# Performance work log

Measured on AMD Instinct MI355X. Metric: run time of the kernel, lower is better.

## Reference

```python
import jax, jax.numpy as jnp
import numpy as np
from jax import lax

B, T, D = 2, 1024, 2048
HK, HV = 8, 16          # num key heads / num value heads
DK, DV = 128, 128       # head dims
KW = 4                  # conv kernel size
EPS = 1e-6
KEY_DIM = HK * DK
VALUE_DIM = HV * DV
CONV_DIM = 2 * KEY_DIM + VALUE_DIM


def setup_inputs() -> dict:
    key = jax.random.key(0)
    ks = jax.random.split(key, 9)
    w = lambda k, shape, s=0.02: jax.random.normal(k, shape, jnp.float32) * s
    return {
        'hidden_states': jax.random.normal(ks[0], (B, T, D), jnp.float32),
        'W_qkv': w(ks[1], (D, CONV_DIM)),
        'W_z': w(ks[2], (D, VALUE_DIM)),
        'W_b': w(ks[3], (D, HV)),
        'W_a': w(ks[4], (D, HV)),
        'conv_w': w(ks[5], (CONV_DIM, KW), 0.5),
        'dt_bias': jnp.ones((HV,), jnp.float32),
        'A_log': jnp.log(jax.random.uniform(ks[6], (HV,), jnp.float32, 1e-3, 16.0)),
        'norm_weight': jnp.ones((DV,), jnp.float32),
        'W_out': w(ks[7], (VALUE_DIM, D)),
    }


def _causal_conv_silu(x, w):
    # x: [B, C, T], w: [C, K] depthwise causal conv + SiLU (causal_conv1d_fn)
    k = w.shape[1]
    xp = jnp.pad(x, ((0, 0), (0, 0), (k - 1, 0)))
    y = sum(w[:, j][None, :, None] * xp[:, :, j:j + x.shape[2]] for j in range(k))
    return jax.nn.silu(y)


def _l2norm(x):
    return x * lax.rsqrt(jnp.sum(x * x, -1, keepdims=True) + 1e-6)


def reference(hidden_states, W_qkv, W_z, W_b, W_a, conv_w, dt_bias, A_log,
              norm_weight, W_out):
    Bb, Tt, _ = hidden_states.shape
    mixed = hidden_states @ W_qkv                       # [B,T,conv_dim]
    mixed = _causal_conv_silu(mixed.transpose(0, 2, 1), conv_w).transpose(0, 2, 1)
    q, k, v = jnp.split(mixed, [KEY_DIM, 2 * KEY_DIM], axis=-1)
    q = q.reshape(Bb, Tt, HK, DK)
    k = k.reshape(Bb, Tt, HK, DK)
    v = v.reshape(Bb, Tt, HV, DV)
    z = (hidden_states @ W_z).reshape(Bb, Tt, HV, DV)
    beta = jax.nn.sigmoid(hidden_states @ W_b)          # [B,T,HV]
    g = -jnp.exp(A_log) * jax.nn.softplus(hidden_states @ W_a + dt_bias)  # [B,T,HV]

    rep = HV // HK  # GQA: repeat_interleave q,k heads
    q = jnp.repeat(q, rep, axis=2)
    k = jnp.repeat(k, rep, axis=2)
    q = _l2norm(q) * (DK ** -0.5)                       # use_qk_l2norm + scale
    k = _l2norm(k)

    # gated delta-rule recurrence (fp32 state), scanned over time
    qs = q.transpose(1, 0, 2, 3)   # [T,B,HV,DK]
    ks = k.transpose(1, 0, 2, 3)
    vs = v.transpose(1, 0, 2, 3)   # [T,B,HV,DV]
    gs = g.transpose(1, 0, 2)      # [T,B,HV]
    bs = beta.transpose(1, 0, 2)

    def step(S, inp):
        qt, kt, vt, gt, bt = inp
        S = S * jnp.exp(gt)[..., None, None]                          # decay
        v_adj = (vt - jnp.einsum('bhk,bhkv->bhv', kt, S)) * bt[..., None]
        S = S + kt[..., None] * v_adj[..., None, :]                   # rank-1 delta update
        o = jnp.einsum('bhk,bhkv->bhv', qt, S)
        return S, o

    S0 = jnp.zeros((Bb, HV, DK, DV), jnp.float32)
    _, o = lax.scan(step, S0, (qs, ks, vs, gs, bs))
    o = o.transpose(1, 0, 2, 3)                         # [B,T,HV,DV]

    # gated RMSNorm over head_v_dim
    var = jnp.mean(o * o, -1, keepdims=True)
    o = o * lax.rsqrt(var + EPS) * norm_weight
    o = o * jax.nn.silu(z)

    return o.reshape(Bb, Tt, VALUE_DIM) @ W_out         # [B,T,D]
```

## Files before the change

kernel.cpp:

```cpp
#include <hip/hip_runtime.h>
#include <hip/hip_bf16.h>

#define B_ 2
#define T_ 1024
#define D_ 2048
#define HK_ 8
#define HV_ 16
#define DK_ 128
#define DV_ 128
#define KEY_DIM_ 1024
#define VALUE_DIM_ 2048
#define CONV_DIM_ 4096
#define BT_ 2048
#define NCH_ 16
#define CL_ 64

typedef __attribute__((ext_vector_type(8))) short short8;
typedef __attribute__((ext_vector_type(4))) float f32x4;

__device__ __forceinline__ short f2bf(float x) {
  __hip_bfloat16 h = __float2bfloat16(x);
  return *reinterpret_cast<short*>(&h);
}
__device__ __forceinline__ float bf2f(short u) {
  unsigned int x = ((unsigned int)(unsigned short)u) << 16;
  return __int_as_float(x);
}

#define GLOAD_LDS16(g, l)                                             \
  __builtin_amdgcn_global_load_lds(                                   \
      (const __attribute__((address_space(1))) void*)(g),             \
      (__attribute__((address_space(3))) void*)(l), 16, 0, 0)

__global__ void cast_plain(const float* __restrict__ in, short* __restrict__ out, int n4) {
  int i = blockIdx.x * blockDim.x + threadIdx.x;
  if (i < n4) {
    float4 v = ((const float4*)in)[i];
    short4 o;
    o.x = f2bf(v.x); o.y = f2bf(v.y); o.z = f2bf(v.z); o.w = f2bf(v.w);
    ((short4*)out)[i] = o;
  }
}

__global__ void transpose_cast(const float* __restrict__ W, short* __restrict__ WT, int R, int C) {
  __shared__ float tile[32][33];
  int tx = threadIdx.x, ty = threadIdx.y;
  int x = blockIdx.x * 32 + tx;
#pragma unroll
  for (int j = 0; j < 4; ++j) {
    int r = blockIdx.y * 32 + ty + j * 8;
    tile[ty + j * 8][tx] = W[(long)r * C + x];
  }
  __syncthreads();
  int ro = blockIdx.y * 32 + tx;
#pragma unroll
  for (int j = 0; j < 4; ++j) {
    int co = blockIdx.x * 32 + ty + j * 8;
    WT[(long)co * R + ro] = f2bf(tile[tx][ty + j * 8]);
  }
}

__global__ void interleave_ba(const float* __restrict__ Wb, const float* __restrict__ Wa,
                              float* __restrict__ Wba32) {
  int i = blockIdx.x * 256 + threadIdx.x;
  int c = i & 31, k = i >> 5;
  Wba32[i] = (c < 16) ? Wb[k * 16 + c] : Wa[k * 16 + (c - 16)];
}

__global__ __launch_bounds__(256) void gemm128_split(const short* __restrict__ A,
                                                     const short* __restrict__ Bt,
                                                     float* __restrict__ C0,
                                                     float* __restrict__ C1,
                                                     int N0, int N1, int K) {
  __shared__ short As[128 * 32];
  __shared__ short Bs[128 * 32];
  int m0 = blockIdx.y * 128, n0 = blockIdx.x * 128;
  int tid = threadIdx.x;
  int wave = tid >> 6, lane = tid & 63;
  int wm = (wave >> 1) * 64, wn = (wave & 1) * 64;
  int quad = lane >> 4, l16 = lane & 15;
  f32x4 acc[4][4] = {};

  int ar = tid >> 2;
  int ac = (tid & 3) * 8;
  const short* Ag0 = A + (long)(m0 + ar) * K + ac;
  const short* Ag1 = A + (long)(m0 + 64 + ar) * K + ac;
  const short* Bg0 = Bt + (long)(n0 + ar) * K + ac;
  const short* Bg1 = Bt + (long)(n0 + 64 + ar) * K + ac;
  short* lA0 = As + tid * 8;
  short* lA1 = As + 64 * 32 + tid * 8;
  short* lB0 = Bs + tid * 8;
  short* lB1 = Bs + 64 * 32 + tid * 8;

  for (int k0 = 0; k0 < K; k0 += 32) {
    GLOAD_LDS16(Ag0 + k0, lA0);
    GLOAD_LDS16(Ag1 + k0, lA1);
    GLOAD_LDS16(Bg0 + k0, lB0);
    GLOAD_LDS16(Bg1 + k0, lB1);
    __syncthreads();

    short8 af[4], bf_[4];
#pragma unroll
    for (int i = 0; i < 4; ++i) af[i] = *(const short8*)(As + (wm + i * 16 + l16) * 32 + quad * 8);
#pragma unroll
    for (int j = 0; j < 4; ++j) bf_[j] = *(const short8*)(Bs + (wn + j * 16 + l16) * 32 + quad * 8);
#pragma unroll
    for (int i = 0; i < 4; ++i)
#pragma unroll
      for (int j = 0; j < 4; ++j)
        acc[i][j] = __builtin_amdgcn_mfma_f32_16x16x32_bf16(af[i], bf_[j], acc[i][j], 0, 0, 0);
    __syncthreads();
  }

  float* Cw; int ldc, cb;
  if (n0 < N0) { Cw = C0; ldc = N0; cb = n0; }
  else         { Cw = C1; ldc = N1; cb = n0 - N0; }
#pragma unroll
  for (int i = 0; i < 4; ++i)
#pragma unroll
    for (int j = 0; j < 4; ++j)
#pragma unroll
      for (int r = 0; r < 4; ++r) {
        int row = m0 + wm + i * 16 + quad * 4 + r;
        int colx = cb + wn + j * 16 + l16;
        Cw[(long)row * ldc + colx] = acc[i][j][r];
      }
}

__global__ __launch_bounds__(256) void gemm128_ks(const short* __restrict__ A,
                                                  const short* __restrict__ Bt,
                                                  float* __restrict__ Cp,
                                                  int M, int N, int K) {
  __shared__ short As[128 * 32];
  __shared__ short Bs[128 * 32];
  int m0 = blockIdx.y * 128, n0 = blockIdx.x * 128;
  int kh = K >> 1;
  int kbeg = blockIdx.z * kh;
  int tid = threadIdx.x;
  int wave = tid >> 6, lane = tid & 63;
  int wm = (wave >> 1) * 64, wn = (wave & 1) * 64;
  int quad = lane >> 4, l16 = lane & 15;
  f32x4 acc[4][4] = {};

  int ar = tid >> 2;
  int ac = (tid & 3) * 8;
  const short* Ag0 = A + (long)(m0 + ar) * K + ac + kbeg;
  const short* Ag1 = A + (long)(m0 + 64 + ar) * K + ac + kbeg;
  const short* Bg0 = Bt + (long)(n0 + ar) * K + ac + kbeg;
  const short* Bg1 = Bt + (long)(n0 + 64 + ar) * K + ac + kbeg;
  short* lA0 = As + tid * 8;
  short* lA1 = As + 64 * 32 + tid * 8;
  short* lB0 = Bs + tid * 8;
  short* lB1 = Bs + 64 * 32 + tid * 8;

  for (int k0 = 0; k0 < kh; k0 += 32) {
    GLOAD_LDS16(Ag0 + k0, lA0);
    GLOAD_LDS16(Ag1 + k0, lA1);
    GLOAD_LDS16(Bg0 + k0, lB0);
    GLOAD_LDS16(Bg1 + k0, lB1);
    __syncthreads();

    short8 af[4], bf_[4];
#pragma unroll
    for (int i = 0; i < 4; ++i) af[i] = *(const short8*)(As + (wm + i * 16 + l16) * 32 + quad * 8);
#pragma unroll
    for (int j = 0; j < 4; ++j) bf_[j] = *(const short8*)(Bs + (wn + j * 16 + l16) * 32 + quad * 8);
#pragma unroll
    for (int i = 0; i < 4; ++i)
#pragma unroll
      for (int j = 0; j < 4; ++j)
        acc[i][j] = __builtin_amdgcn_mfma_f32_16x16x32_bf16(af[i], bf_[j], acc[i][j], 0, 0, 0);
    __syncthreads();
  }

  float* Cz = Cp + (long)blockIdx.z * M * N;
#pragma unroll
  for (int i = 0; i < 4; ++i)
#pragma unroll
    for (int j = 0; j < 4; ++j)
#pragma unroll
      for (int r = 0; r < 4; ++r) {
        int row = m0 + wm + i * 16 + quad * 4 + r;
        int colx = n0 + wn + j * 16 + l16;
        Cz[(long)row * N + colx] = acc[i][j][r];
      }
}

__global__ void add2(const float* __restrict__ p0, const float* __restrict__ p1,
                     float* __restrict__ out, int n4) {
  int i = blockIdx.x * 256 + threadIdx.x;
  if (i < n4) {
    float4 a = ((const float4*)p0)[i];
    float4 b = ((const float4*)p1)[i];
    float4 o;
    o.x = a.x + b.x; o.y = a.y + b.y; o.z = a.z + b.z; o.w = a.w + b.w;
    ((float4*)out)[i] = o;
  }
}

__global__ __launch_bounds__(256) void small_proj(const float* __restrict__ hidden,
                                                  const float* __restrict__ Wba32,
                                                  const float* __restrict__ dt_bias,
                                                  const float* __restrict__ A_log,
                                                  float* __restrict__ betaT,
                                                  float* __restrict__ gT) {
  __shared__ float red[2][32][33];
  int r0 = blockIdx.x * 2;
  int tid = threadIdx.x;
  int cg = tid & 7, s = tid >> 3;
  const f32x4* wp = (const f32x4*)Wba32 + (long)s * 64 * 8 + cg;
  const f32x4* h0 = (const f32x4*)(hidden + (long)r0 * D_ + s * 64);
  const f32x4* h1 = (const f32x4*)(hidden + (long)(r0 + 1) * D_ + s * 64);
  f32x4 a0 = {0.f, 0.f, 0.f, 0.f}, a1 = {0.f, 0.f, 0.f, 0.f};
#pragma unroll
  for (int ii = 0; ii < 16; ++ii) {
    f32x4 ha = h0[ii], hb = h1[ii];
    f32x4 w0 = wp[(ii * 4 + 0) * 8];
    f32x4 w1 = wp[(ii * 4 + 1) * 8];
    f32x4 w2 = wp[(ii * 4 + 2) * 8];
    f32x4 w3 = wp[(ii * 4 + 3) * 8];
    a0 += ha[0] * w0; a1 += hb[0] * w0;
    a0 += ha[1] * w1; a1 += hb[1] * w1;
    a0 += ha[2] * w2; a1 += hb[2] * w2;
    a0 += ha[3] * w3; a1 += hb[3] * w3;
  }
#pragma unroll
  for (int j = 0; j < 4; ++j) {
    red[0][s][cg * 4 + j] = a0[j];
    red[1][s][cg * 4 + j] = a1[j];
  }
  __syncthreads();
  if (tid < 64) {
    int row = tid >> 5, c = tid & 31;
    float t0 = 0.f, t1 = 0.f, t2 = 0.f, t3 = 0.f;
#pragma unroll
    for (int ss = 0; ss < 32; ss += 4) {
      t0 += red[row][ss][c];
      t1 += red[row][ss + 1][c];
      t2 += red[row][ss + 2][c];
      t3 += red[row][ss + 3][c];
    }
    float t = (t0 + t1) + (t2 + t3);
    int r = r0 + row;
    if (c < 16) {
      betaT[c * BT_ + r] = 1.f / (1.f + __expf(-t));
    } else {
      int hh = c - 16;
      float y = t + dt_bias[hh];
      float sp = fmaxf(y, 0.f) + log1pf(__expf(-fabsf(y)));
      gT[hh * BT_ + r] = -__expf(A_log[hh]) * sp;
    }
  }
}

__global__ void conv_silu(const float* __restrict__ x, const float* __restrict__ w,
                          float* __restrict__ y) {
  int idx = blockIdx.x * 256 + threadIdx.x;
  int c = idx & (CONV_DIM_ - 1);
  int bt = idx >> 12;
  int t = bt & (T_ - 1);
  float4 wc = *(const float4*)(w + c * 4);
  const float* xp = x + (long)idx;
  float acc = wc.w * xp[0];
  if (t >= 1) acc += wc.z * xp[-CONV_DIM_];
  if (t >= 2) acc += wc.y * xp[-2 * CONV_DIM_];
  if (t >= 3) acc += wc.x * xp[-3 * CONV_DIM_];
  y[idx] = acc * (1.f / (1.f + __expf(-acc)));
}

__global__ __launch_bounds__(64) void qknorm(const float* __restrict__ qkv,
                                             short* __restrict__ qb, short* __restrict__ kb) {
  int bi = blockIdx.x;
  int which = bi & 1;
  int h = (bi >> 1) & 7;
  int bt = bi >> 4;
  int lane = threadIdx.x;
  const float* src = qkv + (long)bt * CONV_DIM_ + which * KEY_DIM_ + h * DK_;
  float2 v = *(const float2*)(src + lane * 2);
  float ss = v.x * v.x + v.y * v.y;
#pragma unroll
  for (int m = 32; m; m >>= 1) ss += __shfl_xor(ss, m, 64);
  float scale = rsqrtf(ss + 1e-6f);
  if (which == 0) scale *= 0.08838834764831845f;
  short* dst = (which ? kb : qb) + ((long)bt * HK_ + h) * DK_;
  short2 o; o.x = f2bf(v.x * scale); o.y = f2bf(v.y * scale);
  ((short2*)dst)[lane] = o;
}

__global__ __launch_bounds__(256, 2) void chunk_phase1(
    const short* __restrict__ qbf, const short* __restrict__ kbf,
    const float* __restrict__ qkv, const float* __restrict__ gT,
    const float* __restrict__ bT,
    short* __restrict__ Pm, short* __restrict__ GQ, short* __restrict__ KtT,
    short* __restrict__ Wneg, float* __restrict__ Ut, float* __restrict__ Gammac) {
  __shared__ float Al[64 * 64];
  __shared__ float Gs[64], Gam[64], Dd[64], Bet[64], BG[64];

  int ci = blockIdx.x;
  int c = ci & 15, hv = (ci >> 4) & 15, b = ci >> 8;
  int hk = hv >> 1;
  int t0 = c * CL_;
  int tid = threadIdx.x;
  int wave = tid >> 6, lane = tid & 63, quad = lane >> 4, l16 = lane & 15;

  if (tid < 64) {
    float g = gT[(hv * B_ + b) * T_ + t0 + tid];
    float x = g;
#pragma unroll
    for (int off = 1; off < 64; off <<= 1) {
      float y = __shfl_up(x, off, 64);
      if (tid >= off) x += y;
    }
    Gs[tid] = x;
    float gm = __expf(x);
    Gam[tid] = gm;
    float Gtot = __shfl(x, 63, 64);
    Dd[tid] = __expf(Gtot - x);
    float bb = bT[(hv * B_ + b) * T_ + t0 + tid];
    Bet[tid] = bb;
    BG[tid] = bb * gm;
    if (tid == 63) Gammac[ci] = __expf(x);
  }
  __syncthreads();

  const long kbase = ((long)(b * T_ + t0) * HK_ + hk) * DK_;
  const int kstride = HK_ * DK_;

  int half = tid >> 7;
  int col = tid & 127;
  float u[64];
  {
    const float* vcol = qkv + (long)(b * T_ + t0) * CONV_DIM_ + 2 * KEY_DIM_ + hv * DV_ + col;
    const short* kcol = kbf + kbase + col;
    if (half == 0) {
#pragma unroll
      for (int r = 0; r < 64; ++r) u[r] = vcol[(long)r * CONV_DIM_];
    } else {
#pragma unroll
      for (int r = 0; r < 64; ++r) u[r] = bf2f(kcol[(long)r * kstride]);
    }
  }

  {
    f32x4 acc[4] = {};
#pragma unroll
    for (int kk = 0; kk < 4; ++kk) {
      short8 afr = *(const short8*)(kbf + kbase + (long)(16 * wave + l16) * kstride + kk * 32 + quad * 8);
#pragma unroll
      for (int j = 0; j < 4; ++j) {
        short8 bfr = *(const short8*)(kbf + kbase + (long)(16 * j + l16) * kstride + kk * 32 + quad * 8);
        acc[j] = __builtin_amdgcn_mfma_f32_16x16x32_bf16(afr, bfr, acc[j], 0, 0, 0);
      }
    }
#pragma unroll
    for (int j = 0; j < 4; ++j)
#pragma unroll
      for (int r = 0; r < 4; ++r) {
        int row = 16 * wave + quad * 4 + r, colx = 16 * j + l16;
        float v = 0.f;
        if (row > colx) v = Bet[row] * __expf(Gs[row] - Gs[colx]) * acc[j][r];
        Al[row * 64 + colx] = v;
      }
  }
  {
    f32x4 acc[4] = {};
#pragma unroll
    for (int kk = 0; kk < 4; ++kk) {
      short8 afr = *(const short8*)(qbf + kbase + (long)(16 * wave + l16) * kstride + kk * 32 + quad * 8);
#pragma unroll
      for (int j = 0; j < 4; ++j) {
        short8 bfr = *(const short8*)(kbf + kbase + (long)(16 * j + l16) * kstride + kk * 32 + quad * 8);
        acc[j] = __builtin_amdgcn_mfma_f32_16x16x32_bf16(afr, bfr, acc[j], 0, 0, 0);
      }
    }
#pragma unroll
    for (int j = 0; j < 4; ++j)
#pragma unroll
      for (int r = 0; r < 4; ++r) {
        int row = 16 * wave + quad * 4 + r, colx = 16 * j + l16;
        float v = 0.f;
        if (row >= colx) v = __expf(Gs[row] - Gs[colx]) * acc[j][r];
        Pm[(long)ci * 4096 + row * 64 + colx] = f2bf(v);
      }
  }
  for (int s = wave; s < 64; s += 4) {
    float gm = Gam[s];
    short2 qv = *(const short2*)(qbf + kbase + (long)s * kstride + lane * 2);
    short2 o;
    o.x = f2bf(bf2f(qv.x) * gm);
    o.y = f2bf(bf2f(qv.y) * gm);
    *(short2*)(GQ + (long)ci * 8192 + s * 128 + lane * 2) = o;
  }
  for (int d = wave; d < 128; d += 4) {
    float kv = bf2f(kbf[kbase + (long)lane * kstride + d]);
    KtT[(long)ci * 8192 + d * 64 + lane] = f2bf(kv * Dd[lane]);
  }
  __syncthreads();

  if (half == 0) {
#pragma unroll
    for (int r = 0; r < 64; ++r) u[r] *= Bet[r];
  } else {
#pragma unroll
    for (int r = 0; r < 64; ++r) u[r] *= BG[r];
  }
#pragma unroll
  for (int s = 1; s < 64; ++s) {
    const float* Ar = Al + s * 64;
    float acc = 0.f;
#pragma unroll
    for (int r4 = 0; r4 + 4 <= s; r4 += 4) {
      float4 a = *(const float4*)(Ar + r4);
      acc += (a.x * u[r4] + a.y * u[r4 + 1]) + (a.z * u[r4 + 2] + a.w * u[r4 + 3]);
    }
#pragma unroll
    for (int r = (s / 4) * 4; r < s; ++r) acc += Ar[r] * u[r];
    u[s] -= acc;
  }
  if (half == 0) {
    float* up = Ut + (long)ci * 8192 + col;
#pragma unroll
    for (int s = 0; s < 64; ++s) up[s * 128] = u[s];
  } else {
    short* wp = Wneg + (long)ci * 8192 + col;
#pragma unroll
    for (int s = 0; s < 64; ++s) wp[s * 128] = f2bf(-u[s]);
  }
}

__global__ __launch_bounds__(256) void chunk_phase2(
    const short* __restrict__ Wneg, const float* __restrict__ Ut,
    const short* __restrict__ KtT, const float* __restrict__ Gammac,
    short* __restrict__ UTg, short* __restrict__ ScTg) {
  __shared__ short SLT[64 * 136];
  __shared__ short ULT[64 * 72];
  int bi = blockIdx.x >> 1;
  int n0 = (blockIdx.x & 1) * 64;
  int tid = threadIdx.x, wave = tid >> 6, lane = tid & 63, quad = lane >> 4, l16 = lane & 15;
  f32x4 S[2][4] = {};

  for (int ch = 0; ch < NCH_; ++ch) {
    long ci = (long)bi * NCH_ + ch;
#pragma unroll
    for (int i = 0; i < 2; ++i)
#pragma unroll
      for (int j = 0; j < 4; ++j) {
        int m0 = 32 * wave + 16 * i + quad * 4;
        int n = 16 * j + l16;
        short4 p;
        p.x = f2bf(S[i][j][0]); p.y = f2bf(S[i][j][1]);
        p.z = f2bf(S[i][j][2]); p.w = f2bf(S[i][j][3]);
        *(short4*)(SLT + n * 136 + m0) = p;
        *(short4*)(ScTg + ci * 16384 + (n0 + n) * 128 + m0) = p;
      }
    __syncthreads();
    f32x4 Ua[4];
#pragma unroll
    for (int j = 0; j < 4; ++j) {
      const float* up = Ut + ci * 8192 + (16 * wave + quad * 4) * 128 + n0 + 16 * j + l16;
#pragma unroll
      for (int r = 0; r < 4; ++r) Ua[j][r] = up[r * 128];
    }
#pragma unroll
    for (int kk = 0; kk < 4; ++kk) {
      short8 af = *(const short8*)(Wneg + ci * 8192 + (16 * wave + l16) * 128 + kk * 32 + quad * 8);
#pragma unroll
      for (int j = 0; j < 4; ++j) {
        short8 bfv = *(const short8*)(SLT + (16 * j + l16) * 136 + kk * 32 + quad * 8);
        Ua[j] = __builtin_amdgcn_mfma_f32_16x16x32_bf16(af, bfv, Ua[j], 0, 0, 0);
      }
    }
#pragma unroll
    for (int j = 0; j < 4; ++j) {
      int n = 16 * j + l16, s0q = 16 * wave + quad * 4;
      short4 p;
      p.x = f2bf(Ua[j][0]); p.y = f2bf(Ua[j][1]);
      p.z = f2bf(Ua[j][2]); p.w = f2bf(Ua[j][3]);
      *(short4*)(ULT + n * 72 + s0q) = p;
      *(short4*)(UTg + ci * 8192 + (n0 + n) * 64 + s0q) = p;
    }
    __syncthreads();
    float gc = Gammac[ci];
#pragma unroll
    for (int i = 0; i < 2; ++i)
#pragma unroll
      for (int j = 0; j < 4; ++j)
#pragma unroll
        for (int r = 0; r < 4; ++r) S[i][j][r] *= gc;
#pragma unroll
    for (int kk = 0; kk < 2; ++kk)
#pragma unroll
      for (int i = 0; i < 2; ++i) {
        short8 af = *(const short8*)(KtT + ci * 8192 + (32 * wave + 16 * i + l16) * 64 + kk * 32 + quad * 8);
#pragma unroll
        for (int j = 0; j < 4; ++j) {
          short8 bfv = *(const short8*)(ULT + (16 * j + l16) * 72 + kk * 32 + quad * 8);
          S[i][j] = __builtin_amdgcn_mfma_f32_16x16x32_bf16(af, bfv, S[i][j], 0, 0, 0);
        }
      }
    __syncthreads();
  }
}

__global__ __launch_bounds__(256) void chunk_phase3(
    const short* __restrict__ GQ, const short* __restrict__ ScTg,
    const short* __restrict__ Pm, const short* __restrict__ UTg,
    const float* __restrict__ zbuf, const float* __restrict__ nw,
    short* __restrict__ obf) {
  int ci = blockIdx.x;
  int c = ci & 15, hv = (ci >> 4) & 15, b = ci >> 8;
  int t0 = c * CL_;
  int tid = threadIdx.x, wave = tid >> 6, lane = tid & 63, quad = lane >> 4, l16 = lane & 15;
  f32x4 acc[8] = {};
#pragma unroll
  for (int kk = 0; kk < 4; ++kk) {
    short8 af = *(const short8*)(GQ + (long)ci * 8192 + (16 * wave + l16) * 128 + kk * 32 + quad * 8);
#pragma unroll
    for (int j = 0; j < 8; ++j) {
      short8 bfv = *(const short8*)(ScTg + (long)ci * 16384 + (16 * j + l16) * 128 + kk * 32 + quad * 8);
      acc[j] = __builtin_amdgcn_mfma_f32_16x16x32_bf16(af, bfv, acc[j], 0, 0, 0);
    }
  }
#pragma unroll
  for (int kk = 0; kk < 2; ++kk) {
    short8 af = *(const short8*)(Pm + (long)ci * 4096 + (16 * wave + l16) * 64 + kk * 32 + quad * 8);
#pragma unroll
    for (int j = 0; j < 8; ++j) {
      short8 bfv = *(const short8*)(UTg + (long)ci * 8192 + (16 * j + l16) * 64 + kk * 32 + quad * 8);
      acc[j] = __builtin_amdgcn_mfma_f32_16x16x32_bf16(af, bfv, acc[j], 0, 0, 0);
    }
  }
#pragma unroll
  for (int r = 0; r < 4; ++r) {
    float ss = 0.f;
#pragma unroll
    for (int j = 0; j < 8; ++j) ss += acc[j][r] * acc[j][r];
    ss += __shfl_xor(ss, 1, 64);
    ss += __shfl_xor(ss, 2, 64);
    ss += __shfl_xor(ss, 4, 64);
    ss += __shfl_xor(ss, 8, 64);
    float scale = rsqrtf(ss * (1.f / 128.f) + 1e-6f);
    int t = t0 + 16 * wave + quad * 4 + r;
    long base = (long)(b * T_ + t) * VALUE_DIM_ + hv * DV_;
#pragma unroll
    for (int j = 0; j < 8; ++j) {
      int n = 16 * j + l16;
      float zv = zbuf[base + n];
      float sz = zv * (1.f / (1.f + __expf(-zv)));
      obf[base + n] = f2bf(acc[j][r] * scale * nw[n] * sz);
    }
  }
}

extern "C" void kernel_launch(void* const* d_in, const int* in_sizes, int n_in,
                              void* d_out, int out_size, void* d_ws, size_t ws_size,
                              hipStream_t stream) {
  const float* hidden  = (const float*)d_in[0];
  const float* W_qkv   = (const float*)d_in[1];
  const float* W_z     = (const float*)d_in[2];
  const float* W_b     = (const float*)d_in[3];
  const float* W_a     = (const float*)d_in[4];
  const float* conv_w  = (const float*)d_in[5];
  const float* dt_bias = (const float*)d_in[6];
  const float* A_log   = (const float*)d_in[7];
  const float* norm_w  = (const float*)d_in[8];
  const float* W_out   = (const float*)d_in[9];
  float* out = (float*)d_out;

  char* ws = (char*)d_ws;
  size_t off = 0;
  auto alloc = [&](size_t bytes) {
    void* p = ws + off;
    off += (bytes + 255) & ~(size_t)255;
    return p;
  };
  short* hidden_bf = (short*)alloc((size_t)BT_ * D_ * 2);
  short* WcatT     = (short*)alloc((size_t)(CONV_DIM_ + VALUE_DIM_) * D_ * 2);
  short* WoutT     = (short*)alloc((size_t)D_ * VALUE_DIM_ * 2);
  float* mixed     = (float*)alloc((size_t)BT_ * CONV_DIM_ * 4);
  float* qkv       = (float*)alloc((size_t)BT_ * CONV_DIM_ * 4);
  float* zbuf      = (float*)alloc((size_t)BT_ * VALUE_DIM_ * 4);
  short* qbf       = (short*)alloc((size_t)BT_ * KEY_DIM_ * 2);
  short* kbf       = (short*)alloc((size_t)BT_ * KEY_DIM_ * 2);
  float* betab     = (float*)alloc((size_t)BT_ * HV_ * 4);
  float* gb        = (float*)alloc((size_t)BT_ * HV_ * 4);
  float* Wba32     = (float*)alloc((size_t)D_ * 32 * 4);
  short* Wneg      = (short*)alloc((size_t)512 * 8192 * 2);
  float* Ut32      = (float*)alloc((size_t)512 * 8192 * 4);
  short* KtT       = (short*)alloc((size_t)512 * 8192 * 2);
  short* UTg       = (short*)alloc((size_t)512 * 8192 * 2);
  short* ScTg      = (short*)alloc((size_t)512 * 16384 * 2);
  float* Gammac    = (float*)alloc((size_t)512 * 4);
  short* Pm   = (short*)(mixed + (size_t)BT_ * VALUE_DIM_);
  short* GQ   = Pm + (size_t)512 * 4096;
  short* obf  = hidden_bf;
  float* Cpart = qkv;

  dim3 tb32(32, 8);
  cast_plain<<<(BT_ * D_ / 4 + 255) / 256, 256, 0, stream>>>(hidden, hidden_bf, BT_ * D_ / 4);
  transpose_cast<<<dim3(CONV_DIM_ / 32, D_ / 32), tb32, 0, stream>>>(W_qkv, WcatT, D_, CONV_DIM_);
  transpose_cast<<<dim3(VALUE_DIM_ / 32, D_ / 32), tb32, 0, stream>>>(W_z, WcatT + (size_t)CONV_DIM_ * D_, D_, VALUE_DIM_);
  transpose_cast<<<dim3(D_ / 32, VALUE_DIM_ / 32), tb32, 0, stream>>>(W_out, WoutT, VALUE_DIM_, D_);
  interleave_ba<<<32 * D_ / 256, 256, 0, stream>>>(W_b, W_a, Wba32);

  gemm128_split<<<dim3((CONV_DIM_ + VALUE_DIM_) / 128, BT_ / 128), 256, 0, stream>>>(
      hidden_bf, WcatT, mixed, zbuf, CONV_DIM_, VALUE_DIM_, D_);
  small_proj<<<BT_ / 2, 256, 0, stream>>>(hidden, Wba32, dt_bias, A_log, betab, gb);
  conv_silu<<<BT_ * CONV_DIM_ / 256, 256, 0, stream>>>(mixed, conv_w, qkv);
  qknorm<<<BT_ * HK_ * 2, 64, 0, stream>>>(qkv, qbf, kbf);

  chunk_phase1<<<512, 256, 0, stream>>>(qbf, kbf, qkv, gb, betab, Pm, GQ, KtT, Wneg, Ut32, Gammac);
  chunk_phase2<<<64, 256, 0, stream>>>(Wneg, Ut32, KtT, Gammac, UTg, ScTg);
  chunk_phase3<<<512, 256, 0, stream>>>(GQ, ScTg, Pm, UTg, zbuf, norm_w, obf);

  gemm128_ks<<<dim3(D_ / 128, BT_ / 128, 2), 256, 0, stream>>>(obf, WoutT, Cpart, BT_, D_, VALUE_DIM_);
  add2<<<(BT_ * D_ / 4 + 255) / 256, 256, 0, stream>>>(Cpart, Cpart + (size_t)BT_ * D_, out, BT_ * D_ / 4);
}
```

Before: 417.9 us.

## Double-buffer GEMM loads, fuse hidden cast into small_proj, widen chunk_phase2 grid

Both GEMM kernels now double-buffer their LDS tiles. Each iteration prefetches tile t+2 while computing on tile t, using explicit vmcnt waits and raw barriers in place of __syncthreads. The standalone fp32-to-bf16 cast of hidden is folded into small_proj, which now runs before the first GEMM, removing one launch and one pass over the input. chunk_phase2 splits the value dimension into 16-column slices across 256 blocks instead of 64, and register-prefetches the next chunk's inputs to cut the serial chunk-loop latency. The cost is double the LDS per GEMM block and redundant reloads of Wneg and KtT across the extra phase2 blocks.

Result: faster. 376.0 us (-10.0%).

```diff
diff --git a/kernel.cpp b/kernel.cpp
--- a/kernel.cpp
+++ b/kernel.cpp
@@ -32,16 +32,6 @@
       (const __attribute__((address_space(1))) void*)(g),             \
       (__attribute__((address_space(3))) void*)(l), 16, 0, 0)
 
-__global__ void cast_plain(const float* __restrict__ in, short* __restrict__ out, int n4) {
-  int i = blockIdx.x * blockDim.x + threadIdx.x;
-  if (i < n4) {
-    float4 v = ((const float4*)in)[i];
-    short4 o;
-    o.x = f2bf(v.x); o.y = f2bf(v.y); o.z = f2bf(v.z); o.w = f2bf(v.w);
-    ((short4*)out)[i] = o;
-  }
-}
-
 __global__ void transpose_cast(const float* __restrict__ W, short* __restrict__ WT, int R, int C) {
   __shared__ float tile[32][33];
   int tx = threadIdx.x, ty = threadIdx.y;
@@ -72,8 +62,8 @@
                                                      float* __restrict__ C0,
                                                      float* __restrict__ C1,
                                                      int N0, int N1, int K) {
-  __shared__ short As[128 * 32];
-  __shared__ short Bs[128 * 32];
+  __shared__ short As[2][128 * 32];
+  __shared__ short Bs[2][128 * 32];
   int m0 = blockIdx.y * 128, n0 = blockIdx.x * 128;
   int tid = threadIdx.x;
   int wave = tid >> 6, lane = tid & 63;
@@ -87,29 +77,43 @@
   const short* Ag1 = A + (long)(m0 + 64 + ar) * K + ac;
   const short* Bg0 = Bt + (long)(n0 + ar) * K + ac;
   const short* Bg1 = Bt + (long)(n0 + 64 + ar) * K + ac;
-  short* lA0 = As + tid * 8;
-  short* lA1 = As + 64 * 32 + tid * 8;
-  short* lB0 = Bs + tid * 8;
-  short* lB1 = Bs + 64 * 32 + tid * 8;
-
-  for (int k0 = 0; k0 < K; k0 += 32) {
-    GLOAD_LDS16(Ag0 + k0, lA0);
-    GLOAD_LDS16(Ag1 + k0, lA1);
-    GLOAD_LDS16(Bg0 + k0, lB0);
-    GLOAD_LDS16(Bg1 + k0, lB1);
-    __syncthreads();
+  int NT = K >> 5;
+
+#define STAGE_(t, c)                                  \
+  do {                                                \
+    GLOAD_LDS16(Ag0 + (t) * 32, As[c] + tid * 8);     \
+    GLOAD_LDS16(Ag1 + (t) * 32, As[c] + 64 * 32 + tid * 8); \
+    GLOAD_LDS16(Bg0 + (t) * 32, Bs[c] + tid * 8);     \
+    GLOAD_LDS16(Bg1 + (t) * 32, Bs[c] + 64 * 32 + tid * 8); \
+  } while (0)
+
+  STAGE_(0, 0);
+  STAGE_(1, 1);
+
+  for (int t = 0; t < NT; ++t) {
+    int c = t & 1;
+    if (t + 1 < NT) {
+      asm volatile("s_waitcnt vmcnt(4)" ::: "memory");
+    } else {
+      asm volatile("s_waitcnt vmcnt(0)" ::: "memory");
+    }
+    __builtin_amdgcn_s_barrier();
+    __builtin_amdgcn_sched_barrier(0);
 
     short8 af[4], bf_[4];
 #pragma unroll
-    for (int i = 0; i < 4; ++i) af[i] = *(const short8*)(As + (wm + i * 16 + l16) * 32 + quad * 8);
-#pragma unroll
-    for (int j = 0; j < 4; ++j) bf_[j] = *(const short8*)(Bs + (wn + j * 16 + l16) * 32 + quad * 8);
+    for (int i = 0; i < 4; ++i) af[i] = *(const short8*)(As[c] + (wm + i * 16 + l16) * 32 + quad * 8);
+#pragma unroll
+    for (int j = 0; j < 4; ++j) bf_[j] = *(const short8*)(Bs[c] + (wn + j * 16 + l16) * 32 + quad * 8);
 #pragma unroll
     for (int i = 0; i < 4; ++i)
 #pragma unroll
       for (int j = 0; j < 4; ++j)
         acc[i][j] = __builtin_amdgcn_mfma_f32_16x16x32_bf16(af[i], bf_[j], acc[i][j], 0, 0, 0);
-    __syncthreads();
+
+    __builtin_amdgcn_sched_barrier(0);
+    __builtin_amdgcn_s_barrier();
+    if (t + 2 < NT) STAGE_(t + 2, c);
   }
 
   float* Cw; int ldc, cb;
@@ -125,14 +129,15 @@
         int colx = cb + wn + j * 16 + l16;
         Cw[(long)row * ldc + colx] = acc[i][j][r];
       }
+#undef STAGE_
 }
 
 __global__ __launch_bounds__(256) void gemm128_ks(const short* __restrict__ A,
                                                   const short* __restrict__ Bt,
                                                   float* __restrict__ Cp,
                                                   int M, int N, int K) {
-  __shared__ short As[128 * 32];
-  __shared__ short Bs[128 * 32];
+  __shared__ short As[2][128 * 32];
+  __shared__ short Bs[2][128 * 32];
   int m0 = blockIdx.y * 128, n0 = blockIdx.x * 128;
   int kh = K >> 1;
   int kbeg = blockIdx.z * kh;
@@ -148,29 +153,43 @@
   const short* Ag1 = A + (long)(m0 + 64 + ar) * K + ac + kbeg;
   const short* Bg0 = Bt + (long)(n0 + ar) * K + ac + kbeg;
   const short* Bg1 = Bt + (long)(n0 + 64 + ar) * K + ac + kbeg;
-  short* lA0 = As + tid * 8;
-  short* lA1 = As + 64 * 32 + tid * 8;
-  short* lB0 = Bs + tid * 8;
-  short* lB1 = Bs + 64 * 32 + tid * 8;
-
-  for (int k0 = 0; k0 < kh; k0 += 32) {
-    GLOAD_LDS16(Ag0 + k0, lA0);
-    GLOAD_LDS16(Ag1 + k0, lA1);
-    GLOAD_LDS16(Bg0 + k0, lB0);
-    GLOAD_LDS16(Bg1 + k0, lB1);
-    __syncthreads();
+  int NT = kh >> 5;
+
+#define STAGE_(t, c)                                  \
+  do {                                                \
+    GLOAD_LDS16(Ag0 + (t) * 32, As[c] + tid * 8);     \
+    GLOAD_LDS16(Ag1 + (t) * 32, As[c] + 64 * 32 + tid * 8); \
+    GLOAD_LDS16(Bg0 + (t) * 32, Bs[c] + tid * 8);     \
+    GLOAD_LDS16(Bg1 + (t) * 32, Bs[c] + 64 * 32 + tid * 8); \
+  } while (0)
+
+  STAGE_(0, 0);
+  STAGE_(1, 1);
+
+  for (int t = 0; t < NT; ++t) {
+    int c = t & 1;
+    if (t + 1 < NT) {
+      asm volatile("s_waitcnt vmcnt(4)" ::: "memory");
+    } else {
+      asm volatile("s_waitcnt vmcnt(0)" ::: "memory");
+    }
+    __builtin_amdgcn_s_barrier();
+    __builtin_amdgcn_sched_barrier(0);
 
     short8 af[4], bf_[4];
 #pragma unroll
-    for (int i = 0; i < 4; ++i) af[i] = *(const short8*)(As + (wm + i * 16 + l16) * 32 + quad * 8);
-#pragma unroll
-    for (int j = 0; j < 4; ++j) bf_[j] = *(const short8*)(Bs + (wn + j * 16 + l16) * 32 + quad * 8);
+    for (int i = 0; i < 4; ++i) af[i] = *(const short8*)(As[c] + (wm + i * 16 + l16) * 32 + quad * 8);
+#pragma unroll
+    for (int j = 0; j < 4; ++j) bf_[j] = *(const short8*)(Bs[c] + (wn + j * 16 + l16) * 32 + quad * 8);
 #pragma unroll
     for (int i = 0; i < 4; ++i)
 #pragma unroll
       for (int j = 0; j < 4; ++j)
         acc[i][j] = __builtin_amdgcn_mfma_f32_16x16x32_bf16(af[i], bf_[j], acc[i][j], 0, 0, 0);
-    __syncthreads();
+
+    __builtin_amdgcn_sched_barrier(0);
+    __builtin_amdgcn_s_barrier();
+    if (t + 2 < NT) STAGE_(t + 2, c);
   }
 
   float* Cz = Cp + (long)blockIdx.z * M * N;
@@ -184,6 +203,7 @@
         int colx = n0 + wn + j * 16 + l16;
         Cz[(long)row * N + colx] = acc[i][j][r];
       }
+#undef STAGE_
 }
 
 __global__ void add2(const float* __restrict__ p0, const float* __restrict__ p1,
@@ -203,7 +223,8 @@
                                                   const float* __restrict__ dt_bias,
                                                   const float* __restrict__ A_log,
                                                   float* __restrict__ betaT,
-                                                  float* __restrict__ gT) {
+                                                  float* __restrict__ gT,
+                                                  short* __restrict__ hbf) {
   __shared__ float red[2][32][33];
   int r0 = blockIdx.x * 2;
   int tid = threadIdx.x;
@@ -228,6 +249,22 @@
   for (int j = 0; j < 4; ++j) {
     red[0][s][cg * 4 + j] = a0[j];
     red[1][s][cg * 4 + j] = a1[j];
+  }
+  {
+    int colb = s * 64 + cg * 8;
+    const float* p0 = hidden + (long)r0 * D_ + colb;
+    const float* p1 = p0 + D_;
+    float4 x0 = *(const float4*)(p0);
+    float4 x1 = *(const float4*)(p0 + 4);
+    float4 y0 = *(const float4*)(p1);
+    float4 y1 = *(const float4*)(p1 + 4);
+    short8 o0, o1;
+    o0[0] = f2bf(x0.x); o0[1] = f2bf(x0.y); o0[2] = f2bf(x0.z); o0[3] = f2bf(x0.w);
+    o0[4] = f2bf(x1.x); o0[5] = f2bf(x1.y); o0[6] = f2bf(x1.z); o0[7] = f2bf(x1.w);
+    o1[0] = f2bf(y0.x); o1[1] = f2bf(y0.y); o1[2] = f2bf(y0.z); o1[3] = f2bf(y0.w);
+    o1[4] = f2bf(y1.x); o1[5] = f2bf(y1.y); o1[6] = f2bf(y1.z); o1[7] = f2bf(y1.w);
+    *(short8*)(hbf + (long)r0 * D_ + colb) = o0;
+    *(short8*)(hbf + (long)(r0 + 1) * D_ + colb) = o1;
   }
   __syncthreads();
   if (tid < 64) {
@@ -432,73 +469,93 @@
     const short* __restrict__ Wneg, const float* __restrict__ Ut,
     const short* __restrict__ KtT, const float* __restrict__ Gammac,
     short* __restrict__ UTg, short* __restrict__ ScTg) {
-  __shared__ short SLT[64 * 136];
-  __shared__ short ULT[64 * 72];
-  int bi = blockIdx.x >> 1;
-  int n0 = (blockIdx.x & 1) * 64;
+  __shared__ short SLT[16 * 136];
+  __shared__ short ULT[16 * 72];
+  int bi = blockIdx.x >> 3;
+  int n0 = (blockIdx.x & 7) * 16;
   int tid = threadIdx.x, wave = tid >> 6, lane = tid & 63, quad = lane >> 4, l16 = lane & 15;
-  f32x4 S[2][4] = {};
+  f32x4 S2[2] = {};
+
+  long ci0 = (long)bi * NCH_;
+  short8 Wr[4]; f32x4 Ur; short8 Kr[2][2];
+  {
+    long ci = ci0;
+#pragma unroll
+    for (int kk = 0; kk < 4; ++kk)
+      Wr[kk] = *(const short8*)(Wneg + ci * 8192 + (16 * wave + l16) * 128 + kk * 32 + quad * 8);
+    const float* up = Ut + ci * 8192 + (16 * wave + quad * 4) * 128 + n0 + l16;
+#pragma unroll
+    for (int r = 0; r < 4; ++r) Ur[r] = up[r * 128];
+#pragma unroll
+    for (int kk = 0; kk < 2; ++kk)
+#pragma unroll
+      for (int i = 0; i < 2; ++i)
+        Kr[kk][i] = *(const short8*)(KtT + ci * 8192 + (32 * wave + 16 * i + l16) * 64 + kk * 32 + quad * 8);
+  }
 
   for (int ch = 0; ch < NCH_; ++ch) {
-    long ci = (long)bi * NCH_ + ch;
-#pragma unroll
-    for (int i = 0; i < 2; ++i)
-#pragma unroll
-      for (int j = 0; j < 4; ++j) {
-        int m0 = 32 * wave + 16 * i + quad * 4;
-        int n = 16 * j + l16;
-        short4 p;
-        p.x = f2bf(S[i][j][0]); p.y = f2bf(S[i][j][1]);
-        p.z = f2bf(S[i][j][2]); p.w = f2bf(S[i][j][3]);
-        *(short4*)(SLT + n * 136 + m0) = p;
-        *(short4*)(ScTg + ci * 16384 + (n0 + n) * 128 + m0) = p;
-      }
+    long ci = ci0 + ch;
+#pragma unroll
+    for (int i = 0; i < 2; ++i) {
+      int m0 = 32 * wave + 16 * i + quad * 4;
+      short4 p;
+      p.x = f2bf(S2[i][0]); p.y = f2bf(S2[i][1]);
+      p.z = f2bf(S2[i][2]); p.w = f2bf(S2[i][3]);
+      *(short4*)(SLT + l16 * 136 + m0) = p;
+      *(short4*)(ScTg + ci * 16384 + (n0 + l16) * 128 + m0) = p;
+    }
+    short8 Wn[4]; f32x4 Un; short8 Kn[2][2];
+    if (ch + 1 < NCH_) {
+      long cj = ci + 1;
+#pragma unroll
+      for (int kk = 0; kk < 4; ++kk)
+        Wn[kk] = *(const short8*)(Wneg + cj * 8192 + (16 * wave + l16) * 128 + kk * 32 + quad * 8);
+      const float* up = Ut + cj * 8192 + (16 * wave + quad * 4) * 128 + n0 + l16;
+#pragma unroll
+      for (int r = 0; r < 4; ++r) Un[r] = up[r * 128];
+#pragma unroll
+      for (int kk = 0; kk < 2; ++kk)
+#pragma unroll
+        for (int i = 0; i < 2; ++i)
+          Kn[kk][i] = *(const short8*)(KtT + cj * 8192 + (32 * wave + 16 * i + l16) * 64 + kk * 32 + quad * 8);
+    }
     __syncthreads();
-    f32x4 Ua[4];
-#pragma unroll
-    for (int j = 0; j < 4; ++j) {
-      const float* up = Ut + ci * 8192 + (16 * wave + quad * 4) * 128 + n0 + 16 * j + l16;
-#pragma unroll
-      for (int r = 0; r < 4; ++r) Ua[j][r] = up[r * 128];
-    }
+    f32x4 Ua = Ur;
 #pragma unroll
     for (int kk = 0; kk < 4; ++kk) {
-      short8 af = *(const short8*)(Wneg + ci * 8192 + (16 * wave + l16) * 128 + kk * 32 + quad * 8);
-#pragma unroll
-      for (int j = 0; j < 4; ++j) {
-        short8 bfv = *(const short8*)(SLT + (16 * j + l16) * 136 + kk * 32 + quad * 8);
-        Ua[j] = __builtin_amdgcn_mfma_f32_16x16x32_bf16(af, bfv, Ua[j], 0, 0, 0);
-      }
-    }
-#pragma unroll
-    for (int j = 0; j < 4; ++j) {
-      int n = 16 * j + l16, s0q = 16 * wave + quad * 4;
+      short8 bfv = *(const short8*)(SLT + l16 * 136 + kk * 32 + quad * 8);
+      Ua = __builtin_amdgcn_mfma_f32_16x16x32_bf16(Wr[kk], bfv, Ua, 0, 0, 0);
+    }
+    {
+      int s0 = 16 * wave + quad * 4;
       short4 p;
-      p.x = f2bf(Ua[j][0]); p.y = f2bf(Ua[j][1]);
-      p.z = f2bf(Ua[j][2]); p.w = f2bf(Ua[j][3]);
-      *(short4*)(ULT + n * 72 + s0q) = p;
-      *(short4*)(UTg + ci * 8192 + (n0 + n) * 64 + s0q) = p;
+      p.x = f2bf(Ua[0]); p.y = f2bf(Ua[1]); p.z = f2bf(Ua[2]); p.w = f2bf(Ua[3]);
+      *(short4*)(ULT + l16 * 72 + s0) = p;
+      *(short4*)(UTg + ci * 8192 + (n0 + l16) * 64 + s0) = p;
     }
     __syncthreads();
     float gc = Gammac[ci];
 #pragma unroll
     for (int i = 0; i < 2; ++i)
 #pragma unroll
-      for (int j = 0; j < 4; ++j)
-#pragma unroll
-        for (int r = 0; r < 4; ++r) S[i][j][r] *= gc;
-#pragma unroll
-    for (int kk = 0; kk < 2; ++kk)
-#pragma unroll
-      for (int i = 0; i < 2; ++i) {
-        short8 af = *(const short8*)(KtT + ci * 8192 + (32 * wave + 16 * i + l16) * 64 + kk * 32 + quad * 8);
-#pragma unroll
-        for (int j = 0; j < 4; ++j) {
-          short8 bfv = *(const short8*)(ULT + (16 * j + l16) * 72 + kk * 32 + quad * 8);
-          S[i][j] = __builtin_amdgcn_mfma_f32_16x16x32_bf16(af, bfv, S[i][j], 0, 0, 0);
-        }
-      }
+      for (int r = 0; r < 4; ++r) S2[i][r] *= gc;
+#pragma unroll
+    for (int kk = 0; kk < 2; ++kk) {
+      short8 bfv = *(const short8*)(ULT + l16 * 72 + kk * 32 + quad * 8);
+#pragma unroll
+      for (int i = 0; i < 2; ++i)
+        S2[i] = __builtin_amdgcn_mfma_f32_16x16x32_bf16(Kr[kk][i], bfv, S2[i], 0, 0, 0);
+    }
     __syncthreads();
+    if (ch + 1 < NCH_) {
+#pragma unroll
+      for (int kk = 0; kk < 4; ++kk) Wr[kk] = Wn[kk];
+      Ur = Un;
+#pragma unroll
+      for (int kk = 0; kk < 2; ++kk)
+#pragma unroll
+        for (int i = 0; i < 2; ++i) Kr[kk][i] = Kn[kk][i];
+    }
   }
 }
 
@@ -597,20 +654,20 @@
   float* Cpart = qkv;
 
   dim3 tb32(32, 8);
-  cast_plain<<<(BT_ * D_ / 4 + 255) / 256, 256, 0, stream>>>(hidden, hidden_bf, BT_ * D_ / 4);
   transpose_cast<<<dim3(CONV_DIM_ / 32, D_ / 32), tb32, 0, stream>>>(W_qkv, WcatT, D_, CONV_DIM_);
   transpose_cast<<<dim3(VALUE_DIM_ / 32, D_ / 32), tb32, 0, stream>>>(W_z, WcatT + (size_t)CONV_DIM_ * D_, D_, VALUE_DIM_);
   transpose_cast<<<dim3(D_ / 32, VALUE_DIM_ / 32), tb32, 0, stream>>>(W_out, WoutT, VALUE_DIM_, D_);
   interleave_ba<<<32 * D_ / 256, 256, 0, stream>>>(W_b, W_a, Wba32);
 
+  small_proj<<<BT_ / 2, 256, 0, stream>>>(hidden, Wba32, dt_bias, A_log, betab, gb, hidden_bf);
+
   gemm128_split<<<dim3((CONV_DIM_ + VALUE_DIM_) / 128, BT_ / 128), 256, 0, stream>>>(
       hidden_bf, WcatT, mixed, zbuf, CONV_DIM_, VALUE_DIM_, D_);
-  small_proj<<<BT_ / 2, 256, 0, stream>>>(hidden, Wba32, dt_bias, A_log, betab, gb);
   conv_silu<<<BT_ * CONV_DIM_ / 256, 256, 0, stream>>>(mixed, conv_w, qkv);
   qknorm<<<BT_ * HK_ * 2, 64, 0, stream>>>(qkv, qbf, kbf);
 
   chunk_phase1<<<512, 256, 0, stream>>>(qbf, kbf, qkv, gb, betab, Pm, GQ, KtT, Wneg, Ut32, Gammac);
-  chunk_phase2<<<64, 256, 0, stream>>>(Wneg, Ut32, KtT, Gammac, UTg, ScTg);
+  chunk_phase2<<<256, 256, 0, stream>>>(Wneg, Ut32, KtT, Gammac, UTg, ScTg);
   chunk_phase3<<<512, 256, 0, stream>>>(GQ, ScTg, Pm, UTg, zbuf, norm_w, obf);
 
   gemm128_ks<<<dim3(D_ / 128, BT_ / 128, 2), 256, 0, stream>>>(obf, WoutT, Cpart, BT_, D_, VALUE_DIM_);
```
